# Optimization experiments

Measured on AMD Instinct MI355X. Metric: run time of the kernel, lower is better.

## Reference

```python
import jax, jax.numpy as jnp
import numpy as np

L = 2048      # target/source sequence length (self-attention)
N = 2         # batch size
E = 256       # embed_dim
H = 8         # num_heads
N_AGENTS = 16


def setup_inputs() -> dict:
    key = jax.random.key(0)
    ks = jax.random.split(key, 9)
    w = 0.02
    ids = jax.random.randint(ks[7], (L,), 0, N_AGENTS, dtype=jnp.int32)
    return {
        "query": jax.random.normal(ks[0], (L, N, E), dtype=jnp.float32),
        "in_proj_weight": jax.random.normal(ks[1], (3 * E, E), dtype=jnp.float32) * w,
        "in_proj_bias": jax.random.normal(ks[2], (3 * E,), dtype=jnp.float32) * w,
        "in_proj_weight_self": jax.random.normal(ks[3], (2 * E, E), dtype=jnp.float32) * w,
        "in_proj_bias_self": jax.random.normal(ks[4], (2 * E,), dtype=jnp.float32) * w,
        "out_proj_weight": jax.random.normal(ks[5], (E, E), dtype=jnp.float32) * w,
        "out_proj_bias": jax.random.normal(ks[6], (E,), dtype=jnp.float32) * w,
        "q_identities": ids,                # self-attention: same identities for q and k
        "k_identities": ids,
    }


def reference(query, in_proj_weight, in_proj_bias, in_proj_weight_self,
              in_proj_bias_self, out_proj_weight, out_proj_bias,
              q_identities, k_identities):
    tgt_len, bsz, embed_dim = query.shape
    head_dim = embed_dim // H
    scaling = jnp.asarray(head_dim, query.dtype) ** -0.5

    # combined in-projection (self-attention fast path), then chunk into q,k,v
    qkv = query @ in_proj_weight.T + in_proj_bias            # (L,N,3E)
    q, k, v = jnp.split(qkv, 3, axis=-1)
    qk_self = query @ in_proj_weight_self.T + in_proj_bias_self  # (L,N,2E)
    q_self, k_self = jnp.split(qk_self, 2, axis=-1)

    q = q * scaling
    q_self = q_self * scaling

    def to_heads(x):  # (L,N,E) -> (N*H, L, head_dim), matching torch view+transpose
        return x.reshape(tgt_len, bsz * H, head_dim).transpose(1, 0, 2)

    q, k, v, q_self, k_self = map(to_heads, (q, k, v, q_self, k_self))

    w_inter = jnp.einsum('bld,bsd->bls', q, k)           # (N*H, L, S)
    w_self = jnp.einsum('bld,bsd->bls', q_self, k_self)  # (N*H, L, S)

    # agent-aware mask: 1 where query/key identities match, broadcast over batch*heads
    mask = (k_identities[None, :] == q_identities[:, None]).astype(query.dtype)  # (L,S)
    attn_weights = w_inter * (1.0 - mask) + w_self * mask

    attn = jax.nn.softmax(attn_weights, axis=-1)
    out = jnp.einsum('bls,bsd->bld', attn, v)            # (N*H, L, head_dim)
    out = out.transpose(1, 0, 2).reshape(tgt_len, bsz, embed_dim)
    out = out @ out_proj_weight.T + out_proj_bias        # (L,N,E)
    return out
```

## Files before the change

kernel.cpp:

```cpp
#include <hip/hip_runtime.h>
#include <hip/hip_bf16.h>

typedef __attribute__((ext_vector_type(8))) short short8b;
typedef __attribute__((ext_vector_type(4))) float float4v;

static __device__ __forceinline__ unsigned short f2bf_bits(float f) {
  union { __hip_bfloat16 h; unsigned short u; } c;
  c.h = __float2bfloat16(f);
  return c.u;
}

static __device__ __forceinline__ short8b cvt8(const float* s) {
  union { short8b v; unsigned short us[8]; } o;
#pragma unroll
  for (int i = 0; i < 8; ++i) o.us[i] = f2bf_bits(s[i]);
  return o.v;
}

__global__ __launch_bounds__(256) void cast_X(const float* __restrict__ src,
                                              __hip_bfloat16* __restrict__ dst) {
  int i = blockIdx.x * 256 + threadIdx.x;
  float4 v = reinterpret_cast<const float4*>(src)[i];
  union { ushort4 u; __hip_bfloat16 h[4]; } o;
  o.h[0] = __float2bfloat16(v.x); o.h[1] = __float2bfloat16(v.y);
  o.h[2] = __float2bfloat16(v.z); o.h[3] = __float2bfloat16(v.w);
  reinterpret_cast<ushort4*>(dst)[i] = o.u;
}

__global__ __launch_bounds__(256) void proj_gemm(
    const __hip_bfloat16* __restrict__ Xb, const float* __restrict__ W1,
    const float* __restrict__ W2,
    const float* __restrict__ bias, const float* __restrict__ bias_s,
    __hip_bfloat16* __restrict__ Qs, __hip_bfloat16* __restrict__ Kg,
    __hip_bfloat16* __restrict__ Vt, __hip_bfloat16* __restrict__ Qf,
    __hip_bfloat16* __restrict__ Kf) {
    __shared__ __hip_bfloat16 At[128][40];
    __shared__ __hip_bfloat16 Bt[128][40];
    const int tid = threadIdx.x;
    const int lane = tid & 63, w = tid >> 6;
    const int ln = lane & 15, kg = lane >> 4;
    const int wr = w >> 1, wc = w & 1;
    const int rowBase = blockIdx.y * 128;
    const int colBase = blockIdx.x * 128;
    const float* Wsrc = (colBase < 768) ? (W1 + (size_t)colBase * 256)
                                        : (W2 + (size_t)(colBase - 768) * 256);
    float4v acc[4][4] = {};

    for (int kt = 0; kt < 8; ++kt) {
        int cid = tid;
#pragma unroll
        for (int p = 0; p < 2; ++p, cid += 256) {
            int row = cid >> 2, c = cid & 3;
            *(short8b*)&At[row][c * 8] =
                *(const short8b*)&Xb[(size_t)(rowBase + row) * 256 + kt * 32 + c * 8];
            float fb[8];
            *(float4*)&fb[0] = *(const float4*)&Wsrc[(size_t)row * 256 + kt * 32 + c * 8];
            *(float4*)&fb[4] = *(const float4*)&Wsrc[(size_t)row * 256 + kt * 32 + c * 8 + 4];
            *(short8b*)&Bt[row][c * 8] = cvt8(fb);
        }
        __syncthreads();
        short8b a[4], b[4];
#pragma unroll
        for (int mi = 0; mi < 4; ++mi) a[mi] = *(const short8b*)&At[wr * 64 + mi * 16 + ln][kg * 8];
#pragma unroll
        for (int nj = 0; nj < 4; ++nj) b[nj] = *(const short8b*)&Bt[wc * 64 + nj * 16 + ln][kg * 8];
#pragma unroll
        for (int mi = 0; mi < 4; ++mi)
#pragma unroll
            for (int nj = 0; nj < 4; ++nj)
                acc[mi][nj] = __builtin_amdgcn_mfma_f32_16x16x32_bf16(a[mi], b[nj], acc[mi][nj], 0, 0, 0);
        __syncthreads();
    }

    const float scaling = 0.17677669529663687f * 1.4426950408889634f;
#pragma unroll
    for (int mi = 0; mi < 4; ++mi) {
#pragma unroll
        for (int nj = 0; nj < 4; ++nj) {
            int j = colBase + wc * 64 + nj * 16 + ln;
            float bj = (j < 768) ? bias[j] : bias_s[j - 768];
#pragma unroll
            for (int r = 0; r < 4; ++r) {
                int row = rowBase + wr * 64 + mi * 16 + kg * 4 + r;
                float val = acc[mi][nj][r] + bj;
                int l = row >> 1, n = row & 1;
                if (j < 256) {
                    int h = j >> 5, d = j & 31;
                    Qs[(((n << 3) + h) * 2048 + l) * 32 + d] = __float2bfloat16(val * scaling);
                } else if (j < 512) {
                    int e = j - 256, h = e >> 5, d = e & 31;
                    Kg[(((n << 3) + h) * 2048 + l) * 32 + d] = __float2bfloat16(val);
                } else if (j < 768) {
                    int e = j - 512, h = e >> 5, d = e & 31;
                    Vt[(((n << 3) + h) * 32 + d) * 2048 + l] = __float2bfloat16(val);
                } else if (j < 1024) {
                    int e = j - 768, h = e >> 5, d = e & 31;
                    Qf[(((n << 3) + h) * 2048 + l) * 32 + d] = __float2bfloat16(val * scaling);
                } else {
                    int e = j - 1024, h = e >> 5, d = e & 31;
                    Kf[(((n << 3) + h) * 2048 + l) * 32 + d] = __float2bfloat16(val);
                }
            }
        }
    }
}

__global__ __launch_bounds__(256, 2) void agent_attn(
    const __hip_bfloat16* __restrict__ Qs, const __hip_bfloat16* __restrict__ Kg,
    const __hip_bfloat16* __restrict__ Vt, const __hip_bfloat16* __restrict__ Qf,
    const __hip_bfloat16* __restrict__ Kf, const int* __restrict__ qid_g,
    const int* __restrict__ kid_g, __hip_bfloat16* __restrict__ Ab) {
  __shared__ __hip_bfloat16 Klds[2][64][36];
  __shared__ __hip_bfloat16 Kslds[2][64][36];
  __shared__ __hip_bfloat16 Vlds[2][32][72];

  const int tid = threadIdx.x;
  const int lane = tid & 63, w = tid >> 6;
  const int ln = lane & 15, kg = lane >> 4;

  const int flat = blockIdx.x;
  const int slot = flat >> 3;
  const int bh = ((flat & 7) << 1) | (slot & 1);
  const int qg = slot >> 1;
  const int q0 = qg * 64 + w * 16;
  const int n = bh >> 3, h = bh & 7;

  const __hip_bfloat16* Qb  = Qs + (size_t)bh * 2048 * 32;
  const __hip_bfloat16* Qfb = Qf + (size_t)bh * 2048 * 32;
  const __hip_bfloat16* Kb  = Kg + (size_t)bh * 2048 * 32;
  const __hip_bfloat16* Ksb = Kf + (size_t)bh * 2048 * 32;
  const __hip_bfloat16* Vb  = Vt + (size_t)bh * 32 * 2048;

  const int krho = tid >> 2, kseg = tid & 3;
  const int ksub = krho >> 4, ki = krho & 15;
  const int gK = ((ki >> 2) << 3) + (ki & 3) + ((ksub & 1) << 5) + ((ksub >> 1) << 2);
  const int vrow = tid >> 3, vseg = tid & 7;

  short8b bQ  = *(const short8b*)&Qb [(q0 + ln) * 32 + kg * 8];
  short8b bQf = *(const short8b*)&Qfb[(q0 + ln) * 32 + kg * 8];
  const int qidq = qid_g[q0 + ln];

  float lacc = 0.f;
  float4v O0 = {0.f, 0.f, 0.f, 0.f}, O1 = {0.f, 0.f, 0.f, 0.f};

  {
    short8b rk = *(const short8b*)&Kb [(size_t)gK * 32 + kseg * 8];
    short8b rs = *(const short8b*)&Ksb[(size_t)gK * 32 + kseg * 8];
    short8b rv = *(const short8b*)&Vb [(size_t)vrow * 2048 + vseg * 8];
    *(short8b*)&Klds [0][krho][kseg * 8] = rk;
    *(short8b*)&Kslds[0][krho][kseg * 8] = rs;
    *(short8b*)&Vlds [0][vrow][vseg * 8] = rv;
  }
  __syncthreads();

  short8b rk, rs, rv;
#pragma unroll 1
  for (int t = 0; t < 32; ++t) {
    const int cur = t & 1;
    const int s0 = t * 64;
    if (t < 31) {
      const int s0n = s0 + 64;
      rk = *(const short8b*)&Kb [(size_t)(s0n + gK) * 32 + kseg * 8];
      rs = *(const short8b*)&Ksb[(size_t)(s0n + gK) * 32 + kseg * 8];
      rv = *(const short8b*)&Vb [(size_t)vrow * 2048 + s0n + vseg * 8];
    }
    const int* ip = kid_g + s0 + kg * 8;
    int4 t0 = *(const int4*)(ip);
    int4 t1 = *(const int4*)(ip + 32);
    int4 t2 = *(const int4*)(ip + 4);
    int4 t3 = *(const int4*)(ip + 36);
    int sd[4][4] = {{t0.x, t0.y, t0.z, t0.w}, {t1.x, t1.y, t1.z, t1.w},
                    {t2.x, t2.y, t2.z, t2.w}, {t3.x, t3.y, t3.z, t3.w}};

    short8b aK[4], aS[4], bV[2][2];
#pragma unroll
    for (int sub = 0; sub < 4; ++sub) {
      aK[sub] = *(const short8b*)&Klds [cur][sub * 16 + ln][kg * 8];
      aS[sub] = *(const short8b*)&Kslds[cur][sub * 16 + ln][kg * 8];
    }
#pragma unroll
    for (int kk = 0; kk < 2; ++kk)
#pragma unroll
      for (int dh = 0; dh < 2; ++dh)
        bV[kk][dh] = *(const short8b*)&Vlds[cur][dh * 16 + ln][kk * 32 + kg * 8];

    float4v ci[4], cs[4];
    float4v z = {0.f, 0.f, 0.f, 0.f};
    __builtin_amdgcn_s_setprio(1);
#pragma unroll
    for (int sub = 0; sub < 4; ++sub) {
      ci[sub] = __builtin_amdgcn_mfma_f32_16x16x32_bf16(aK[sub], bQ,  z, 0, 0, 0);
      cs[sub] = __builtin_amdgcn_mfma_f32_16x16x32_bf16(aS[sub], bQf, z, 0, 0, 0);
    }
    __builtin_amdgcn_s_setprio(0);
    float p[4][4];
#pragma unroll
    for (int sub = 0; sub < 4; ++sub)
#pragma unroll
      for (int r = 0; r < 4; ++r)
        p[sub][r] = exp2f((sd[sub][r] == qidq) ? cs[sub][r] : ci[sub][r]);
    float y0 = (p[0][0] + p[0][1]) + (p[0][2] + p[0][3]);
    float y1 = (p[1][0] + p[1][1]) + (p[1][2] + p[1][3]);
    float y2 = (p[2][0] + p[2][1]) + (p[2][2] + p[2][3]);
    float y3 = (p[3][0] + p[3][1]) + (p[3][2] + p[3][3]);
    lacc += (y0 + y1) + (y2 + y3);
    union { short8b v; unsigned short us[8]; } apk[2];
#pragma unroll
    for (int kk = 0; kk < 2; ++kk) {
      apk[kk].us[0] = f2bf_bits(p[kk][0]);     apk[kk].us[1] = f2bf_bits(p[kk][1]);
      apk[kk].us[2] = f2bf_bits(p[kk][2]);     apk[kk].us[3] = f2bf_bits(p[kk][3]);
      apk[kk].us[4] = f2bf_bits(p[kk + 2][0]); apk[kk].us[5] = f2bf_bits(p[kk + 2][1]);
      apk[kk].us[6] = f2bf_bits(p[kk + 2][2]); apk[kk].us[7] = f2bf_bits(p[kk + 2][3]);
    }
    __builtin_amdgcn_s_setprio(1);
#pragma unroll
    for (int kk = 0; kk < 2; ++kk) {
      O0 = __builtin_amdgcn_mfma_f32_16x16x32_bf16(apk[kk].v, bV[kk][0], O0, 0, 0, 0);
      O1 = __builtin_amdgcn_mfma_f32_16x16x32_bf16(apk[kk].v, bV[kk][1], O1, 0, 0, 0);
    }
    __builtin_amdgcn_s_setprio(0);

    if (t < 31) {
      *(short8b*)&Klds [cur ^ 1][krho][kseg * 8] = rk;
      *(short8b*)&Kslds[cur ^ 1][krho][kseg * 8] = rs;
      *(short8b*)&Vlds [cur ^ 1][vrow][vseg * 8] = rv;
    }
    __syncthreads();
  }

  float ps = lacc;
  ps += __shfl_xor(ps, 16);
  ps += __shfl_xor(ps, 32);
  float inv = 1.0f / ps;
#pragma unroll
  for (int r = 0; r < 4; ++r) {
    float s_r = __shfl(inv, kg * 4 + r);
    int q = q0 + kg * 4 + r;
    size_t rowo = ((size_t)q * 2 + n) * 256 + h * 32;
    Ab[rowo + ln]      = __float2bfloat16(O0[r] * s_r);
    Ab[rowo + 16 + ln] = __float2bfloat16(O1[r] * s_r);
  }
}

__global__ __launch_bounds__(256) void out_gemm(
    const __hip_bfloat16* __restrict__ A, const float* __restrict__ Wo,
    const float* __restrict__ bias, float* __restrict__ out) {
    __shared__ __hip_bfloat16 At[64][40];
    __shared__ __hip_bfloat16 Bt[64][40];
    const int tid = threadIdx.x;
    const int lane = tid & 63, w = tid >> 6;
    const int ln = lane & 15, kg = lane >> 4;
    const int wr = w >> 1, wc = w & 1;
    const int rowBase = blockIdx.y * 64;
    const int colBase = blockIdx.x * 64;
    float4v acc[2][2] = {};

    for (int kt = 0; kt < 8; ++kt) {
        int row = tid >> 2, c = tid & 3;
        *(short8b*)&At[row][c * 8] =
            *(const short8b*)&A[(size_t)(rowBase + row) * 256 + kt * 32 + c * 8];
        float fb[8];
        *(float4*)&fb[0] = *(const float4*)&Wo[(size_t)(colBase + row) * 256 + kt * 32 + c * 8];
        *(float4*)&fb[4] = *(const float4*)&Wo[(size_t)(colBase + row) * 256 + kt * 32 + c * 8 + 4];
        *(short8b*)&Bt[row][c * 8] = cvt8(fb);
        __syncthreads();
        short8b a[2], b[2];
#pragma unroll
        for (int mi = 0; mi < 2; ++mi) a[mi] = *(const short8b*)&At[wr * 32 + mi * 16 + ln][kg * 8];
#pragma unroll
        for (int nj = 0; nj < 2; ++nj) b[nj] = *(const short8b*)&Bt[wc * 32 + nj * 16 + ln][kg * 8];
#pragma unroll
        for (int mi = 0; mi < 2; ++mi)
#pragma unroll
            for (int nj = 0; nj < 2; ++nj)
                acc[mi][nj] = __builtin_amdgcn_mfma_f32_16x16x32_bf16(a[mi], b[nj], acc[mi][nj], 0, 0, 0);
        __syncthreads();
    }

#pragma unroll
    for (int mi = 0; mi < 2; ++mi) {
#pragma unroll
        for (int nj = 0; nj < 2; ++nj) {
            int j = colBase + wc * 32 + nj * 16 + ln;
            float bj = bias[j];
#pragma unroll
            for (int r = 0; r < 4; ++r) {
                int row = rowBase + wr * 32 + mi * 16 + kg * 4 + r;
                out[row * 256 + j] = acc[mi][nj][r] + bj;
            }
        }
    }
}

extern "C" void kernel_launch(void* const* d_in, const int* in_sizes, int n_in,
                              void* d_out, int out_size, void* d_ws, size_t ws_size,
                              hipStream_t stream) {
    const float* query = (const float*)d_in[0];
    const float* W_in  = (const float*)d_in[1];
    const float* b_in  = (const float*)d_in[2];
    const float* W_s   = (const float*)d_in[3];
    const float* b_s   = (const float*)d_in[4];
    const float* W_o   = (const float*)d_in[5];
    const float* b_o   = (const float*)d_in[6];
    const int*   qids  = (const int*)d_in[7];
    const int*   kids  = (const int*)d_in[8];
    float* out = (float*)d_out;

    __hip_bfloat16* Qs  = (__hip_bfloat16*)d_ws;
    __hip_bfloat16* Kg  = Qs + 16 * 2048 * 32;
    __hip_bfloat16* Vt  = Kg + 16 * 2048 * 32;
    __hip_bfloat16* Qf  = Vt + 16 * 2048 * 32;
    __hip_bfloat16* Kf  = Qf + 16 * 2048 * 32;
    __hip_bfloat16* Ab  = Kf + 16 * 2048 * 32;
    __hip_bfloat16* Xb  = Ab + 4096 * 256;

    cast_X<<<1024, 256, 0, stream>>>(query, Xb);
    proj_gemm<<<dim3(10, 32), 256, 0, stream>>>(Xb, W_in, W_s, b_in, b_s,
                                                Qs, Kg, Vt, Qf, Kf);
    agent_attn<<<512, 256, 0, stream>>>(Qs, Kg, Vt, Qf, Kf, qids, kids, Ab);
    out_gemm<<<dim3(4, 64), 256, 0, stream>>>(Ab, W_o, b_o, out);
}
```

Baseline: 68.81 us.

## Split attention over key halves with combine kernel; halve projection tile width

The attention kernel now splits the 2048 keys into two halves, launching twice as many blocks. Each block writes unnormalised fp32 partial outputs and row sums, which a new combine kernel adds and normalises into the bf16 attention output. The projection GEMM's column tile shrinks from 128 to 64 so twice as many blocks run. Both changes aim to fill more compute units on the MI355X, at the cost of an extra kernel launch, extra fp32 global traffic for the partials, and less data reuse per projection tile. The combine skips max-rescaling, which relies on the original kernel using no running max.

```diff
diff --git a/kernel.cpp b/kernel.cpp
--- a/kernel.cpp
+++ b/kernel.cpp
@@ -35,16 +35,16 @@
     __hip_bfloat16* __restrict__ Vt, __hip_bfloat16* __restrict__ Qf,
     __hip_bfloat16* __restrict__ Kf) {
     __shared__ __hip_bfloat16 At[128][40];
-    __shared__ __hip_bfloat16 Bt[128][40];
+    __shared__ __hip_bfloat16 Bt[64][40];
     const int tid = threadIdx.x;
     const int lane = tid & 63, w = tid >> 6;
     const int ln = lane & 15, kg = lane >> 4;
     const int wr = w >> 1, wc = w & 1;
     const int rowBase = blockIdx.y * 128;
-    const int colBase = blockIdx.x * 128;
+    const int colBase = blockIdx.x * 64;
     const float* Wsrc = (colBase < 768) ? (W1 + (size_t)colBase * 256)
                                         : (W2 + (size_t)(colBase - 768) * 256);
-    float4v acc[4][4] = {};
+    float4v acc[4][2] = {};
 
     for (int kt = 0; kt < 8; ++kt) {
         int cid = tid;
@@ -53,21 +53,24 @@
             int row = cid >> 2, c = cid & 3;
             *(short8b*)&At[row][c * 8] =
                 *(const short8b*)&Xb[(size_t)(rowBase + row) * 256 + kt * 32 + c * 8];
+        }
+        {
+            int row = tid >> 2, c = tid & 3;
             float fb[8];
             *(float4*)&fb[0] = *(const float4*)&Wsrc[(size_t)row * 256 + kt * 32 + c * 8];
             *(float4*)&fb[4] = *(const float4*)&Wsrc[(size_t)row * 256 + kt * 32 + c * 8 + 4];
             *(short8b*)&Bt[row][c * 8] = cvt8(fb);
         }
         __syncthreads();
-        short8b a[4], b[4];
+        short8b a[4], b[2];
 #pragma unroll
         for (int mi = 0; mi < 4; ++mi) a[mi] = *(const short8b*)&At[wr * 64 + mi * 16 + ln][kg * 8];
 #pragma unroll
-        for (int nj = 0; nj < 4; ++nj) b[nj] = *(const short8b*)&Bt[wc * 64 + nj * 16 + ln][kg * 8];
+        for (int nj = 0; nj < 2; ++nj) b[nj] = *(const short8b*)&Bt[wc * 32 + nj * 16 + ln][kg * 8];
 #pragma unroll
         for (int mi = 0; mi < 4; ++mi)
 #pragma unroll
-            for (int nj = 0; nj < 4; ++nj)
+            for (int nj = 0; nj < 2; ++nj)
                 acc[mi][nj] = __builtin_amdgcn_mfma_f32_16x16x32_bf16(a[mi], b[nj], acc[mi][nj], 0, 0, 0);
         __syncthreads();
     }
@@ -76,8 +79,8 @@
 #pragma unroll
     for (int mi = 0; mi < 4; ++mi) {
 #pragma unroll
-        for (int nj = 0; nj < 4; ++nj) {
-            int j = colBase + wc * 64 + nj * 16 + ln;
+        for (int nj = 0; nj < 2; ++nj) {
+            int j = colBase + wc * 32 + nj * 16 + ln;
             float bj = (j < 768) ? bias[j] : bias_s[j - 768];
 #pragma unroll
             for (int r = 0; r < 4; ++r) {
@@ -109,7 +112,7 @@
     const __hip_bfloat16* __restrict__ Qs, const __hip_bfloat16* __restrict__ Kg,
     const __hip_bfloat16* __restrict__ Vt, const __hip_bfloat16* __restrict__ Qf,
     const __hip_bfloat16* __restrict__ Kf, const int* __restrict__ qid_g,
-    const int* __restrict__ kid_g, __hip_bfloat16* __restrict__ Ab) {
+    const int* __restrict__ kid_g, float* __restrict__ PO, float* __restrict__ PL) {
   __shared__ __hip_bfloat16 Klds[2][64][36];
   __shared__ __hip_bfloat16 Kslds[2][64][36];
   __shared__ __hip_bfloat16 Vlds[2][32][72];
@@ -121,9 +124,10 @@
   const int flat = blockIdx.x;
   const int slot = flat >> 3;
   const int bh = ((flat & 7) << 1) | (slot & 1);
-  const int qg = slot >> 1;
+  const int rest = slot >> 1;
+  const int qg = rest & 31, split = rest >> 5;
   const int q0 = qg * 64 + w * 16;
-  const int n = bh >> 3, h = bh & 7;
+  const int kbase = split * 1024;
 
   const __hip_bfloat16* Qb  = Qs + (size_t)bh * 2048 * 32;
   const __hip_bfloat16* Qfb = Qf + (size_t)bh * 2048 * 32;
@@ -144,9 +148,9 @@
   float4v O0 = {0.f, 0.f, 0.f, 0.f}, O1 = {0.f, 0.f, 0.f, 0.f};
 
   {
-    short8b rk = *(const short8b*)&Kb [(size_t)gK * 32 + kseg * 8];
-    short8b rs = *(const short8b*)&Ksb[(size_t)gK * 32 + kseg * 8];
-    short8b rv = *(const short8b*)&Vb [(size_t)vrow * 2048 + vseg * 8];
+    short8b rk = *(const short8b*)&Kb [(size_t)(kbase + gK) * 32 + kseg * 8];
+    short8b rs = *(const short8b*)&Ksb[(size_t)(kbase + gK) * 32 + kseg * 8];
+    short8b rv = *(const short8b*)&Vb [(size_t)vrow * 2048 + kbase + vseg * 8];
     *(short8b*)&Klds [0][krho][kseg * 8] = rk;
     *(short8b*)&Kslds[0][krho][kseg * 8] = rs;
     *(short8b*)&Vlds [0][vrow][vseg * 8] = rv;
@@ -155,10 +159,10 @@
 
   short8b rk, rs, rv;
 #pragma unroll 1
-  for (int t = 0; t < 32; ++t) {
+  for (int t = 0; t < 16; ++t) {
     const int cur = t & 1;
-    const int s0 = t * 64;
-    if (t < 31) {
+    const int s0 = kbase + t * 64;
+    if (t < 15) {
       const int s0n = s0 + 64;
       rk = *(const short8b*)&Kb [(size_t)(s0n + gK) * 32 + kseg * 8];
       rs = *(const short8b*)&Ksb[(size_t)(s0n + gK) * 32 + kseg * 8];
@@ -220,7 +224,7 @@
     }
     __builtin_amdgcn_s_setprio(0);
 
-    if (t < 31) {
+    if (t < 15) {
       *(short8b*)&Klds [cur ^ 1][krho][kseg * 8] = rk;
       *(short8b*)&Kslds[cur ^ 1][krho][kseg * 8] = rs;
       *(short8b*)&Vlds [cur ^ 1][vrow][vseg * 8] = rv;
@@ -231,15 +235,35 @@
   float ps = lacc;
   ps += __shfl_xor(ps, 16);
   ps += __shfl_xor(ps, 32);
-  float inv = 1.0f / ps;
+  float* pob = PO + (size_t)(split * 16 + bh) * 2048 * 32;
+  float* plb = PL + (size_t)(split * 16 + bh) * 2048;
 #pragma unroll
   for (int r = 0; r < 4; ++r) {
-    float s_r = __shfl(inv, kg * 4 + r);
     int q = q0 + kg * 4 + r;
-    size_t rowo = ((size_t)q * 2 + n) * 256 + h * 32;
-    Ab[rowo + ln]      = __float2bfloat16(O0[r] * s_r);
-    Ab[rowo + 16 + ln] = __float2bfloat16(O1[r] * s_r);
+    pob[(size_t)q * 32 + ln]      = O0[r];
+    pob[(size_t)q * 32 + 16 + ln] = O1[r];
   }
+  if (kg == 0) plb[q0 + ln] = ps;
+}
+
+__global__ __launch_bounds__(256) void combine_splits(
+    const float* __restrict__ PO, const float* __restrict__ PL,
+    __hip_bfloat16* __restrict__ Ab) {
+  const int blk = blockIdx.x;
+  const int bh = blk >> 6;
+  const int q = ((blk & 63) << 5) | (threadIdx.x >> 3);
+  const int d4 = threadIdx.x & 7;
+  const int n = bh >> 3, h = bh & 7;
+  float L = PL[(size_t)bh * 2048 + q] + PL[(size_t)(16 + bh) * 2048 + q];
+  float inv = 1.f / L;
+  float4 a0 = *(const float4*)&PO[((size_t)bh * 2048 + q) * 32 + d4 * 4];
+  float4 a1 = *(const float4*)&PO[((size_t)(16 + bh) * 2048 + q) * 32 + d4 * 4];
+  union { ushort4 u; __hip_bfloat16 hh[4]; } o;
+  o.hh[0] = __float2bfloat16((a0.x + a1.x) * inv);
+  o.hh[1] = __float2bfloat16((a0.y + a1.y) * inv);
+  o.hh[2] = __float2bfloat16((a0.z + a1.z) * inv);
+  o.hh[3] = __float2bfloat16((a0.w + a1.w) * inv);
+  *(ushort4*)&Ab[((size_t)q * 2 + n) * 256 + h * 32 + d4 * 4] = o.u;
 }
 
 __global__ __launch_bounds__(256) void out_gemm(
@@ -313,10 +337,13 @@
     __hip_bfloat16* Kf  = Qf + 16 * 2048 * 32;
     __hip_bfloat16* Ab  = Kf + 16 * 2048 * 32;
     __hip_bfloat16* Xb  = Ab + 4096 * 256;
+    float* PO = (float*)(Xb + 4096 * 256);
+    float* PL = PO + (size_t)2 * 16 * 2048 * 32;
 
     cast_X<<<1024, 256, 0, stream>>>(query, Xb);
-    proj_gemm<<<dim3(10, 32), 256, 0, stream>>>(Xb, W_in, W_s, b_in, b_s,
+    proj_gemm<<<dim3(20, 32), 256, 0, stream>>>(Xb, W_in, W_s, b_in, b_s,
                                                 Qs, Kg, Vt, Qf, Kf);
-    agent_attn<<<512, 256, 0, stream>>>(Qs, Kg, Vt, Qf, Kf, qids, kids, Ab);
+    agent_attn<<<1024, 256, 0, stream>>>(Qs, Kg, Vt, Qf, Kf, qids, kids, PO, PL);
+    combine_splits<<<1024, 256, 0, stream>>>(PO, PL, Ab);
     out_gemm<<<dim3(4, 64), 256, 0, stream>>>(Ab, W_o, b_o, out);
 }
```

Result: faster. 64.88 us (-5.7%).
